# Performance work log

Measured on AMD Instinct MI355X. Metric: run time of the kernel, lower is better.

Reference implementation:

```python
import jax, jax.numpy as jnp
import numpy as np

SCALE = 1.0  # args.scale


def setup_inputs() -> dict:
    key = jax.random.key(0)
    k1, k2, k3, k4, k5 = jax.random.split(key, 5)
    B, S, D, R, LR = 4, 2048, 2048, 2048, 16  # batch, seq, column(emb), row(out), lora rank
    inp = jax.random.normal(k1, (B, S, D), dtype=jnp.float32)
    weight = jax.random.normal(k2, (R, D), dtype=jnp.float32) * (1.0 / np.sqrt(D))
    bias = jax.random.normal(k3, (R,), dtype=jnp.float32)
    lora_right = jax.random.normal(k4, (B, D, LR), dtype=jnp.float32) * 0.02
    lora_left = jax.random.normal(k5, (B, LR, R), dtype=jnp.float32) * 0.02
    return {"input": inp, "weight": weight, "bias": bias,
            "lora_right": lora_right, "lora_left": lora_left}


def reference(input, weight, bias, lora_right, lora_left):
    # Base linear: x @ W^T + b  -> [B, S, R]
    x = jnp.einsum('bsd,rd->bsr', input, weight) + bias
    # Per-sample low-rank LoRA chain: (input @ right) @ left, batched
    t = jnp.einsum('bsd,bdk->bsk', input, lora_right)   # [B, S, LR]
    y = jnp.einsum('bsk,bkr->bsr', t, lora_left)        # [B, S, R]
    # L2-normalize each token vector along the last dim, then scale
    y = y / jnp.linalg.norm(y, axis=-1, keepdims=True)
    y = y * SCALE
    return x + y
```

## Files before the change

### kernel.cpp

```cpp
#include <hip/hip_runtime.h>
#include <hip/hip_bf16.h>

#define SCALE_V 1.0f

typedef __bf16 bf16v8 __attribute__((ext_vector_type(8)));
typedef float f32v4 __attribute__((ext_vector_type(4)));

typedef const __attribute__((address_space(1))) void* gas_t;
typedef __attribute__((address_space(3))) void* las_t;
#define ASYNC_COPY16(g, l) \
    __builtin_amdgcn_global_load_lds((gas_t)(g), (las_t)(l), 16, 0, 0)
#define FENCE() asm volatile("" ::: "memory")
#define MFMA __builtin_amdgcn_mfma_f32_16x16x32_bf16

__global__ __launch_bounds__(256) void transpose_lr_kernel(
    const float* __restrict__ lright, __bf16* __restrict__ lrT) {
    __shared__ float tile[16][273];
    const int b = blockIdx.y;
    const int d0 = blockIdx.x * 256;
    const int t = threadIdx.x;
    const float* src = lright + (size_t)b * 32768 + (size_t)d0 * 16;
    #pragma unroll
    for (int j = 0; j < 16; ++j) {
        tile[t & 15][j * 16 + (t >> 4)] = src[j * 256 + t];
    }
    __syncthreads();
    const int k = t >> 4, dcol = t & 15;
    __bf16* dst = lrT + (size_t)b * 32768 + (size_t)k * 2048 + d0;
    #pragma unroll
    for (int j = 0; j < 16; ++j) {
        dst[dcol + j * 16] = (__bf16)tile[k][dcol + j * 16];
    }
}

__global__ __launch_bounds__(256, 4) void prep_kernel(
    const float* __restrict__ inp, const float* __restrict__ wgt,
    const __bf16* __restrict__ lrT, const float* __restrict__ lleft,
    __bf16* __restrict__ abf, __bf16* __restrict__ wbf,
    float* __restrict__ tout, float* __restrict__ gpart) {
    __shared__ float sm[256];
    const int bid = blockIdx.x;
    const int tid = threadIdx.x;

    if (bid < 2048) {
        const int row0 = bid * 4;
        const int b = row0 >> 11;
        const __bf16* lt = lrT + (size_t)b * 32768;

        float x[4][8];
        #pragma unroll
        for (int rr = 0; rr < 4; ++rr) {
            const float* p = inp + (size_t)(row0 + rr) * 2048 + tid * 8;
            float4 a0 = *(const float4*)p;
            float4 a1 = *(const float4*)(p + 4);
            x[rr][0] = a0.x; x[rr][1] = a0.y; x[rr][2] = a0.z; x[rr][3] = a0.w;
            x[rr][4] = a1.x; x[rr][5] = a1.y; x[rr][6] = a1.z; x[rr][7] = a1.w;
            bf16v8 v;
            #pragma unroll
            for (int i = 0; i < 8; ++i) v[i] = (__bf16)x[rr][i];
            *(bf16v8*)(abf + (size_t)(row0 + rr) * 2048 + tid * 8) = v;
        }

        float v[64];
        #pragma unroll
        for (int k = 0; k < 16; ++k) {
            bf16v8 lb = *(const bf16v8*)(lt + (size_t)k * 2048 + tid * 8);
            float lv[8];
            #pragma unroll
            for (int i = 0; i < 8; ++i) lv[i] = (float)lb[i];
            #pragma unroll
            for (int rr = 0; rr < 4; ++rr) {
                float s = 0.f;
                #pragma unroll
                for (int i = 0; i < 8; ++i) s += x[rr][i] * lv[i];
                v[rr * 16 + k] = s;
            }
        }

        const int lane = tid & 63;
        const int w = tid >> 6;
        #pragma unroll
        for (int s = 1, cnt = 64; s < 64; s <<= 1, cnt >>= 1) {
            const int half = cnt >> 1;
            const bool up = (lane & s) != 0;
            #pragma unroll
            for (int i = 0; i < 32; ++i) {
                if (i < half) {
                    float keep = up ? v[i + half] : v[i];
                    float give = up ? v[i] : v[i + half];
                    v[i] = keep + __shfl_xor(give, s, 64);
                }
            }
        }
        const int rev = ((lane & 1) << 5) | ((lane & 2) << 3) | ((lane & 4) << 1) |
                        ((lane & 8) >> 1) | ((lane & 16) >> 3) | ((lane & 32) >> 5);
        sm[w * 64 + rev] = v[0];
        __syncthreads();
        if (tid < 64) {
            tout[(size_t)row0 * 16 + tid] =
                sm[tid] + sm[64 + tid] + sm[128 + tid] + sm[192 + tid];
        }
    } else if (bid < 4096) {
        const int i = ((bid - 2048) * 256 + tid) * 8;
        float4 x0 = *(const float4*)(wgt + i);
        float4 x1 = *(const float4*)(wgt + i + 4);
        bf16v8 v;
        v[0] = (__bf16)x0.x; v[1] = (__bf16)x0.y; v[2] = (__bf16)x0.z; v[3] = (__bf16)x0.w;
        v[4] = (__bf16)x1.x; v[5] = (__bf16)x1.y; v[6] = (__bf16)x1.z; v[7] = (__bf16)x1.w;
        *(bf16v8*)(wbf + i) = v;
    } else {
        const int g = bid - 4096;
        const int b = g >> 3, c = g & 7;
        const int k = tid >> 4, j = tid & 15;
        const float* pk = lleft + ((size_t)b * 16 + k) * 2048 + c * 256;
        const float* pj = lleft + ((size_t)b * 16 + j) * 2048 + c * 256;
        float s = 0.f;
        #pragma unroll 4
        for (int r = 0; r < 256; r += 4) {
            float4 a = *(const float4*)(pk + r);
            float4 d = *(const float4*)(pj + r);
            s += a.x * d.x + a.y * d.y + a.z * d.z + a.w * d.w;
        }
        gpart[((size_t)b * 8 + c) * 256 + tid] = s;
    }
}

__global__ __launch_bounds__(512, 2) void gemm_ep_kernel(
    const __bf16* __restrict__ abf, const __bf16* __restrict__ wbf,
    const float* __restrict__ bias, const float* __restrict__ traw,
    const float* __restrict__ gpart, const float* __restrict__ lleft,
    float* __restrict__ out) {
    __shared__ __attribute__((aligned(16))) char smem[131072];

    const int tid  = threadIdx.x;
    const int w    = tid >> 6;
    const int lane = tid & 63;
    const int l3   = lane >> 3, l7 = lane & 7;
    const int wm   = w >> 2;
    const int wn   = w & 3;
    const int fr   = lane & 15;

    const int xcd   = blockIdx.x & 7;
    const int local = blockIdx.x >> 3;
    const int tile_n = local & 7;
    const int tile_m = (xcd << 2) | (local >> 3);
    const int row0 = tile_m * 256;
    const int col0 = tile_n * 256;

    const int cswz = ((l7 ^ l3) * 8);
    const size_t aG0 = (size_t)(row0 + 8 * w + l3) * 2048 + cswz;
    const int bCh = 64 * (w >> 2) + 8 * (w & 3);
    const size_t bG0 = (size_t)(col0 + bCh + l3) * 2048 + cswz;
    char* const aDst = smem + 8 * w * 128 + lane * 16;
    char* const bDst = smem + 65536 + bCh * 128 + lane * 16;

#define STAGE_A(BUFOFF, S, KKEL)                                                         \
    do {                                                                                 \
        ASYNC_COPY16(abf + aG0 + (size_t)((S)*64) * 2048 + (KKEL),  aDst + (BUFOFF) + (S)*8192);          \
        ASYNC_COPY16(abf + aG0 + (size_t)((S)*64 + 128) * 2048 + (KKEL), aDst + (BUFOFF) + (S)*8192 + 16384); \
    } while (0)
#define STAGE_B(BUFOFF, S, KKEL)                                                         \
    do {                                                                                 \
        ASYNC_COPY16(wbf + bG0 + (size_t)((S)*32) * 2048 + (KKEL),  bDst + (BUFOFF) + (S)*4096);          \
        ASYNC_COPY16(wbf + bG0 + (size_t)((S)*32 + 128) * 2048 + (KKEL), bDst + (BUFOFF) + (S)*4096 + 16384); \
    } while (0)

    const int kx0 = (((lane >> 4) * 16) ^ (l7 << 4));
    const int kx1 = ((64 + (lane >> 4) * 16) ^ (l7 << 4));
    const char* const aRd = smem + (wm * 128 + fr) * 128;
    const char* const bRd = smem + 65536 + (wn * 64 + fr) * 128;

    f32v4 acc[8][4];
    #pragma unroll
    for (int m = 0; m < 8; ++m)
        #pragma unroll
        for (int n = 0; n < 4; ++n) {
            acc[m][n][0] = 0.f; acc[m][n][1] = 0.f;
            acc[m][n][2] = 0.f; acc[m][n][3] = 0.f;
        }

    STAGE_A(0, 0, 0);
    STAGE_B(0, 0, 0);
    STAGE_B(0, 1, 0);
    STAGE_A(0, 1, 0);
    STAGE_B(32768, 0, 64);
    STAGE_B(32768, 1, 64);
    STAGE_A(32768, 0, 64);
    asm volatile("s_waitcnt vmcnt(6)" ::: "memory");
    FENCE(); __builtin_amdgcn_s_barrier(); FENCE();

    #pragma unroll 2
    for (int kt = 0; kt < 32; ++kt) {
        const int bo = (kt & 1) * 32768;
        const int bn = bo ^ 32768;
        const size_t kk1 = (size_t)((kt + 1) & 31) * 64;
        const size_t kk2 = (size_t)((kt + 2) & 31) * 64;
        bf16v8 af[4][2], bl[2][2], bh[2][2];

        #pragma unroll
        for (int m = 0; m < 4; ++m) {
            af[m][0] = *(const bf16v8*)(aRd + bo + m * 2048 + kx0);
            af[m][1] = *(const bf16v8*)(aRd + bo + m * 2048 + kx1);
        }
        #pragma unroll
        for (int n = 0; n < 2; ++n) {
            bl[n][0] = *(const bf16v8*)(bRd + bo + n * 2048 + kx0);
            bl[n][1] = *(const bf16v8*)(bRd + bo + n * 2048 + kx1);
        }
        STAGE_A(bn, 1, kk1);
        FENCE(); __builtin_amdgcn_s_barrier(); FENCE();
        __builtin_amdgcn_s_setprio(1);
        #pragma unroll
        for (int m = 0; m < 4; ++m)
            #pragma unroll
            for (int n = 0; n < 2; ++n) {
                acc[m][n] = MFMA(af[m][0], bl[n][0], acc[m][n], 0, 0, 0);
                acc[m][n] = MFMA(af[m][1], bl[n][1], acc[m][n], 0, 0, 0);
            }
        __builtin_amdgcn_s_setprio(0);
        FENCE(); __builtin_amdgcn_s_barrier(); FENCE();

        #pragma unroll
        for (int n = 0; n < 2; ++n) {
            bh[n][0] = *(const bf16v8*)(bRd + bo + (n + 2) * 2048 + kx0);
            bh[n][1] = *(const bf16v8*)(bRd + bo + (n + 2) * 2048 + kx1);
        }
        STAGE_B(bo, 0, kk2);
        FENCE(); __builtin_amdgcn_s_barrier(); FENCE();
        __builtin_amdgcn_s_setprio(1);
        #pragma unroll
        for (int m = 0; m < 4; ++m)
            #pragma unroll
            for (int n = 0; n < 2; ++n) {
                acc[m][n + 2] = MFMA(af[m][0], bh[n][0], acc[m][n + 2], 0, 0, 0);
                acc[m][n + 2] = MFMA(af[m][1], bh[n][1], acc[m][n + 2], 0, 0, 0);
            }
        __builtin_amdgcn_s_setprio(0);
        FENCE(); __builtin_amdgcn_s_barrier(); FENCE();

        #pragma unroll
        for (int m = 0; m < 4; ++m) {
            af[m][0] = *(const bf16v8*)(aRd + bo + (m + 4) * 2048 + kx0);
            af[m][1] = *(const bf16v8*)(aRd + bo + (m + 4) * 2048 + kx1);
        }
        STAGE_B(bo, 1, kk2);
        FENCE(); __builtin_amdgcn_s_barrier(); FENCE();
        __builtin_amdgcn_s_setprio(1);
        #pragma unroll
        for (int m = 0; m < 4; ++m)
            #pragma unroll
            for (int n = 0; n < 2; ++n) {
                acc[m + 4][n + 2] = MFMA(af[m][0], bh[n][0], acc[m + 4][n + 2], 0, 0, 0);
                acc[m + 4][n + 2] = MFMA(af[m][1], bh[n][1], acc[m + 4][n + 2], 0, 0, 0);
            }
        __builtin_amdgcn_s_setprio(0);
        FENCE(); __builtin_amdgcn_s_barrier(); FENCE();

        STAGE_A(bo, 0, kk2);
        asm volatile("s_waitcnt vmcnt(6)" ::: "memory");
        FENCE(); __builtin_amdgcn_s_barrier(); FENCE();
        __builtin_amdgcn_s_setprio(1);
        #pragma unroll
        for (int m = 0; m < 4; ++m)
            #pragma unroll
            for (int n = 0; n < 2; ++n) {
                acc[m + 4][n] = MFMA(af[m][0], bl[n][0], acc[m + 4][n], 0, 0, 0);
                acc[m + 4][n] = MFMA(af[m][1], bl[n][1], acc[m + 4][n], 0, 0, 0);
            }
        __builtin_amdgcn_s_setprio(0);
        FENCE(); __builtin_amdgcn_s_barrier(); FENCE();
    }

    asm volatile("s_waitcnt vmcnt(0)" ::: "memory");
    __syncthreads();
    {
        bf16v8 zv;
        #pragma unroll
        for (int i = 0; i < 8; ++i) zv[i] = (__bf16)0.f;

        __bf16* tE  = (__bf16*)smem;
        __bf16* LE  = (__bf16*)(smem + 20480);
        float*  gsf = (float*)(smem + 40960);
        const int bb = row0 >> 11;

        if (tid < 256) {
            float g = 0.f;
            #pragma unroll
            for (int c = 0; c < 8; ++c) g += gpart[((size_t)bb * 8 + c) * 256 + tid];
            gsf[tid] = g;
        }
        {
            const int r = tid >> 1;
            const int h = (tid & 1) * 8;
            const float* lp = lleft + ((size_t)bb * 16 + h) * 2048 + col0 + r;
            bf16v8 lv;
            #pragma unroll
            for (int i = 0; i < 8; ++i) lv[i] = (__bf16)lp[(size_t)i * 2048];
            *(bf16v8*)(LE + r * 40 + h) = lv;
            *(bf16v8*)(LE + r * 40 + 16 + h) = zv;
        }
        __syncthreads();
        if (tid < 256) {
            const float* tp = traw + (size_t)(row0 + tid) * 16;
            float4 a0 = *(const float4*)(tp);
            float4 a1 = *(const float4*)(tp + 4);
            float4 a2 = *(const float4*)(tp + 8);
            float4 a3 = *(const float4*)(tp + 12);
            float tv[16] = {a0.x, a0.y, a0.z, a0.w, a1.x, a1.y, a1.z, a1.w,
                            a2.x, a2.y, a2.z, a2.w, a3.x, a3.y, a3.z, a3.w};
            float q = 0.f;
            #pragma unroll
            for (int k = 0; k < 16; ++k) {
                float s = 0.f;
                #pragma unroll
                for (int j = 0; j < 16; ++j) s += gsf[k * 16 + j] * tv[j];
                q += tv[k] * s;
            }
            const float sc = SCALE_V * rsqrtf(q);
            bf16v8 t0v, t1v;
            #pragma unroll
            for (int i = 0; i < 8; ++i) {
                t0v[i] = (__bf16)(tv[i] * sc);
                t1v[i] = (__bf16)(tv[8 + i] * sc);
            }
            *(bf16v8*)(tE + tid * 40)      = t0v;
            *(bf16v8*)(tE + tid * 40 + 8)  = t1v;
            *(bf16v8*)(tE + tid * 40 + 16) = zv;
            *(bf16v8*)(tE + tid * 40 + 24) = zv;
        }
        __syncthreads();
    }
    {
        const __bf16* tE = (const __bf16*)smem;
        const __bf16* LE = (const __bf16*)(smem + 20480);
        const int ko = (lane >> 4) * 8;
        bf16v8 bE[4];
        #pragma unroll
        for (int n = 0; n < 4; ++n)
            bE[n] = *(const bf16v8*)(LE + (wn * 64 + n * 16 + fr) * 40 + ko);
        #pragma unroll
        for (int m = 0; m < 8; ++m) {
            bf16v8 aE = *(const bf16v8*)(tE + (wm * 128 + m * 16 + fr) * 40 + ko);
            #pragma unroll
            for (int n = 0; n < 4; ++n)
                acc[m][n] = MFMA(aE, bE[n], acc[m][n], 0, 0, 0);
        }
    }

    #pragma unroll
    for (int n = 0; n < 4; ++n) {
        const int gc = col0 + wn * 64 + n * 16 + fr;
        const float bv = bias[gc];
        #pragma unroll
        for (int m = 0; m < 8; ++m) {
            #pragma unroll
            for (int j = 0; j < 4; ++j) {
                const int gr = row0 + wm * 128 + m * 16 + (lane >> 4) * 4 + j;
                out[(size_t)gr * 2048 + gc] = acc[m][n][j] + bv;
            }
        }
    }
#undef STAGE_A
#undef STAGE_B
}

extern "C" void kernel_launch(void* const* d_in, const int* in_sizes, int n_in,
                              void* d_out, int out_size, void* d_ws, size_t ws_size,
                              hipStream_t stream) {
    const float* inp  = (const float*)d_in[0];
    const float* wgt  = (const float*)d_in[1];
    const float* bias = (const float*)d_in[2];
    const float* lrt  = (const float*)d_in[3];
    const float* llf  = (const float*)d_in[4];
    float* out = (float*)d_out;

    char* ws = (char*)d_ws;
    __bf16* abf  = (__bf16*)ws;
    __bf16* wbf  = (__bf16*)(ws + 33554432);
    float*  tbuf = (float*)(ws + 41943040);
    float*  gprt = (float*)(ws + 42467328);
    __bf16* lrT  = (__bf16*)(ws + 42500096);

    transpose_lr_kernel<<<dim3(8, 4), 256, 0, stream>>>(lrt, lrT);
    prep_kernel<<<4128, 256, 0, stream>>>(inp, wgt, lrT, llf, abf, wbf, tbuf, gprt);
    gemm_ep_kernel<<<dim3(256), 512, 0, stream>>>(abf, wbf, bias, tbuf, gprt, llf, out);
}
```

Measured before the change: 104.7 us.

## Restructure GEMM main loop to cut barriers per k-tile and reorder fragment loads

Rewrites the k-loop schedule so all B fragments for the tile are read up front and A fragments are split into two register sets, so each k-step needs fewer workgroup barriers. MFMA quadrants are reordered so each async LDS stage is issued right after the data it overwrites has been read. This is meant to reduce barrier stalls between MFMA phases. In exchange it raises register pressure and depends on a subtle LDS hazard ordering, where any mistake could race on the double buffer.

```diff
diff --git a/kernel.cpp b/kernel.cpp
--- a/kernel.cpp
+++ b/kernel.cpp
@@ -195,79 +195,72 @@
         const int bn = bo ^ 32768;
         const size_t kk1 = (size_t)((kt + 1) & 31) * 64;
         const size_t kk2 = (size_t)((kt + 2) & 31) * 64;
-        bf16v8 af[4][2], bl[2][2], bh[2][2];
+        bf16v8 afA[4][2], afB[4][2], bl[2][2], bh[2][2];
 
         #pragma unroll
         for (int m = 0; m < 4; ++m) {
-            af[m][0] = *(const bf16v8*)(aRd + bo + m * 2048 + kx0);
-            af[m][1] = *(const bf16v8*)(aRd + bo + m * 2048 + kx1);
+            afA[m][0] = *(const bf16v8*)(aRd + bo + m * 2048 + kx0);
+            afA[m][1] = *(const bf16v8*)(aRd + bo + m * 2048 + kx1);
         }
         #pragma unroll
         for (int n = 0; n < 2; ++n) {
             bl[n][0] = *(const bf16v8*)(bRd + bo + n * 2048 + kx0);
             bl[n][1] = *(const bf16v8*)(bRd + bo + n * 2048 + kx1);
+            bh[n][0] = *(const bf16v8*)(bRd + bo + (n + 2) * 2048 + kx0);
+            bh[n][1] = *(const bf16v8*)(bRd + bo + (n + 2) * 2048 + kx1);
         }
         STAGE_A(bn, 1, kk1);
-        FENCE(); __builtin_amdgcn_s_barrier(); FENCE();
         __builtin_amdgcn_s_setprio(1);
         #pragma unroll
         for (int m = 0; m < 4; ++m)
             #pragma unroll
             for (int n = 0; n < 2; ++n) {
-                acc[m][n] = MFMA(af[m][0], bl[n][0], acc[m][n], 0, 0, 0);
-                acc[m][n] = MFMA(af[m][1], bl[n][1], acc[m][n], 0, 0, 0);
+                acc[m][n] = MFMA(afA[m][0], bl[n][0], acc[m][n], 0, 0, 0);
+                acc[m][n] = MFMA(afA[m][1], bl[n][1], acc[m][n], 0, 0, 0);
             }
         __builtin_amdgcn_s_setprio(0);
         FENCE(); __builtin_amdgcn_s_barrier(); FENCE();
 
-        #pragma unroll
-        for (int n = 0; n < 2; ++n) {
-            bh[n][0] = *(const bf16v8*)(bRd + bo + (n + 2) * 2048 + kx0);
-            bh[n][1] = *(const bf16v8*)(bRd + bo + (n + 2) * 2048 + kx1);
+        __builtin_amdgcn_s_setprio(1);
+        #pragma unroll
+        for (int m = 0; m < 4; ++m)
+            #pragma unroll
+            for (int n = 0; n < 2; ++n) {
+                acc[m][n + 2] = MFMA(afA[m][0], bh[n][0], acc[m][n + 2], 0, 0, 0);
+                acc[m][n + 2] = MFMA(afA[m][1], bh[n][1], acc[m][n + 2], 0, 0, 0);
+            }
+        __builtin_amdgcn_s_setprio(0);
+        #pragma unroll
+        for (int m = 0; m < 4; ++m) {
+            afB[m][0] = *(const bf16v8*)(aRd + bo + (m + 4) * 2048 + kx0);
+            afB[m][1] = *(const bf16v8*)(aRd + bo + (m + 4) * 2048 + kx1);
         }
         STAGE_B(bo, 0, kk2);
         FENCE(); __builtin_amdgcn_s_barrier(); FENCE();
+
         __builtin_amdgcn_s_setprio(1);
         #pragma unroll
         for (int m = 0; m < 4; ++m)
             #pragma unroll
             for (int n = 0; n < 2; ++n) {
-                acc[m][n + 2] = MFMA(af[m][0], bh[n][0], acc[m][n + 2], 0, 0, 0);
-                acc[m][n + 2] = MFMA(af[m][1], bh[n][1], acc[m][n + 2], 0, 0, 0);
+                acc[m + 4][n + 2] = MFMA(afB[m][0], bh[n][0], acc[m + 4][n + 2], 0, 0, 0);
+                acc[m + 4][n + 2] = MFMA(afB[m][1], bh[n][1], acc[m + 4][n + 2], 0, 0, 0);
             }
         __builtin_amdgcn_s_setprio(0);
-        FENCE(); __builtin_amdgcn_s_barrier(); FENCE();
-
-        #pragma unroll
-        for (int m = 0; m < 4; ++m) {
-            af[m][0] = *(const bf16v8*)(aRd + bo + (m + 4) * 2048 + kx0);
-            af[m][1] = *(const bf16v8*)(aRd + bo + (m + 4) * 2048 + kx1);
-        }
         STAGE_B(bo, 1, kk2);
         FENCE(); __builtin_amdgcn_s_barrier(); FENCE();
+
         __builtin_amdgcn_s_setprio(1);
         #pragma unroll
         for (int m = 0; m < 4; ++m)
             #pragma unroll
             for (int n = 0; n < 2; ++n) {
-                acc[m + 4][n + 2] = MFMA(af[m][0], bh[n][0], acc[m + 4][n + 2], 0, 0, 0);
-                acc[m + 4][n + 2] = MFMA(af[m][1], bh[n][1], acc[m + 4][n + 2], 0, 0, 0);
+                acc[m + 4][n] = MFMA(afB[m][0], bl[n][0], acc[m + 4][n], 0, 0, 0);
+                acc[m + 4][n] = MFMA(afB[m][1], bl[n][1], acc[m + 4][n], 0, 0, 0);
             }
         __builtin_amdgcn_s_setprio(0);
-        FENCE(); __builtin_amdgcn_s_barrier(); FENCE();
-
         STAGE_A(bo, 0, kk2);
         asm volatile("s_waitcnt vmcnt(6)" ::: "memory");
-        FENCE(); __builtin_amdgcn_s_barrier(); FENCE();
-        __builtin_amdgcn_s_setprio(1);
-        #pragma unroll
-        for (int m = 0; m < 4; ++m)
-            #pragma unroll
-            for (int n = 0; n < 2; ++n) {
-                acc[m + 4][n] = MFMA(af[m][0], bl[n][0], acc[m + 4][n], 0, 0, 0);
-                acc[m + 4][n] = MFMA(af[m][1], bl[n][1], acc[m + 4][n], 0, 0, 0);
-            }
-        __builtin_amdgcn_s_setprio(0);
         FENCE(); __builtin_amdgcn_s_barrier(); FENCE();
     }
 
```

New measurement: 103.6 us, median of 3. No clear change (-1.0%).
